# Kernel tuning notes

Hardware: AMD Instinct MI355X
Metric: run time of the kernel (lower is better)

## Reference

```python
import jax, jax.numpy as jnp
import numpy as np

GCN_DIM, GEO_DIM, HIDDEN_DIM, TOWER_DIM, RECENT_K = 128, 32, 256, 128, 50
NUM_ITEMS, NUM_USERS = 100000, 16384


def _normalize(x, eps=1e-12):
    # torch F.normalize(dim=1): x / max(||x||, eps)
    n = jnp.linalg.norm(x, axis=1, keepdims=True)
    return x / jnp.maximum(n, eps)


def setup_inputs() -> dict:
    key = jax.random.key(0)
    ks = jax.random.split(key, 16)
    s = 0.05  # weight init scale
    return {
        "item_feat": jax.random.normal(ks[0], (NUM_ITEMS, 2), jnp.float32),
        "gcn_item_emb": jax.random.normal(ks[1], (NUM_ITEMS, GCN_DIM), jnp.float32),
        "gcn_user_emb": jax.random.normal(ks[2], (NUM_USERS, GCN_DIM), jnp.float32),
        "user_items": jax.random.randint(ks[3], (NUM_USERS, RECENT_K), 0, NUM_ITEMS, jnp.int32),
        "Wg": s * jax.random.normal(ks[4], (2, GEO_DIM), jnp.float32),
        "bg": jnp.zeros((GEO_DIM,), jnp.float32),
        "Wi1": s * jax.random.normal(ks[5], (GCN_DIM + GEO_DIM, HIDDEN_DIM), jnp.float32),
        "bi1": jnp.zeros((HIDDEN_DIM,), jnp.float32),
        "Wi2": s * jax.random.normal(ks[6], (HIDDEN_DIM, TOWER_DIM), jnp.float32),
        "bi2": jnp.zeros((TOWER_DIM,), jnp.float32),
        "Wq": s * jax.random.normal(ks[7], (GCN_DIM, TOWER_DIM), jnp.float32),
        "bq": jnp.zeros((TOWER_DIM,), jnp.float32),
        "Wk": s * jax.random.normal(ks[8], (TOWER_DIM, TOWER_DIM), jnp.float32),
        "bk": jnp.zeros((TOWER_DIM,), jnp.float32),
        "Wu1": s * jax.random.normal(ks[9], (GCN_DIM + TOWER_DIM, HIDDEN_DIM), jnp.float32),
        "bu1": jnp.zeros((HIDDEN_DIM,), jnp.float32),
        "Wu2": s * jax.random.normal(ks[10], (HIDDEN_DIM, TOWER_DIM), jnp.float32),
        "bu2": jnp.zeros((TOWER_DIM,), jnp.float32),
    }


def reference(item_feat, gcn_item_emb, gcn_user_emb, user_items,
              Wg, bg, Wi1, bi1, Wi2, bi2, Wq, bq, Wk, bk, Wu1, bu1, Wu2, bu2):
    # ---- encode_items ----
    geo = jax.nn.relu(item_feat @ Wg + bg)                       # [I, GEO]
    xi = jnp.concatenate([geo, gcn_item_emb], axis=1)            # [I, GEO+GCN]
    item_emb = _normalize(jax.nn.relu(xi @ Wi1 + bi1) @ Wi2 + bi2)  # [I, T]

    # ---- encode_users (batched ragged attention pooling) ----
    h = item_emb[user_items]                                     # [U, K, T] gather
    q = gcn_user_emb @ Wq + bq                                   # [U, T]
    k = h @ Wk + bk                                              # [U, K, T]
    scores = jnp.einsum('ut,ukt->uk', q, k)                      # [U, K]
    alpha = jax.nn.softmax(scores, axis=1)                       # softmax over history
    rep = jnp.einsum('uk,ukt->ut', alpha, h)                     # [U, T]
    fused = jnp.concatenate([gcn_user_emb, rep], axis=1)         # [U, GCN+T]
    user_emb = _normalize(jax.nn.relu(fused @ Wu1 + bu1) @ Wu2 + bu2)  # [U, T]

    return jnp.concatenate([item_emb, user_emb], axis=0)         # [I+U, T]
```

## Files before the change

kernel.cpp:

```cpp
#include <hip/hip_runtime.h>
#include <hip/hip_bf16.h>
#include <math.h>

#define NITEMS 100000
#define NUSERS 16384
#define GCN 128
#define GEO 32
#define HIDD 256
#define TD 128
#define RK 50

typedef unsigned int uint;
typedef unsigned short ushort;
typedef __bf16 bf16x8 __attribute__((ext_vector_type(8)));
typedef float f32x4 __attribute__((ext_vector_type(4)));

__device__ __forceinline__ ushort bfb(float x) {
  union { __hip_bfloat16 b; ushort u; } t; t.b = __float2bfloat16(x); return t.u;
}
__device__ __forceinline__ uint packbf2(float a, float b) {
  return (uint)bfb(a) | ((uint)bfb(b) << 16);
}
__device__ __forceinline__ float bflo(uint d) { return __uint_as_float(d << 16); }
__device__ __forceinline__ float bfhi(uint d) { return __uint_as_float(d & 0xffff0000u); }

union U4B { uint4 u; bf16x8 b; };
__device__ __forceinline__ bf16x8 ldfrag(const ushort* p) { U4B t; t.u = *(const uint4*)p; return t.b; }
__device__ __forceinline__ bf16x8 pack8c(float4 a0, float4 a1) {
  bf16x8 r;
  r[0] = (__bf16)a0.x; r[1] = (__bf16)a0.y; r[2] = (__bf16)a0.z; r[3] = (__bf16)a0.w;
  r[4] = (__bf16)a1.x; r[5] = (__bf16)a1.y; r[6] = (__bf16)a1.z; r[7] = (__bf16)a1.w;
  return r;
}

__global__ __launch_bounds__(256) void prep_all(
    const float* __restrict__ Wi1, const float* __restrict__ Wi2,
    const float* __restrict__ Wu1, const float* __restrict__ Wu2,
    const float* __restrict__ Wq, const float* __restrict__ Wk,
    const float* __restrict__ bq, const float* __restrict__ gcn_item,
    ushort* __restrict__ Wi1P, ushort* __restrict__ Wi2P,
    ushort* __restrict__ Wu1P, ushort* __restrict__ Wu2P,
    float* __restrict__ WqkS, float* __restrict__ bqk,
    ushort* __restrict__ gitemT)
{
  int id = blockIdx.x * 256 + threadIdx.x;
  if (id < 40960) {
    int k = id >> 8, c = id & 255;
    Wi1P[(k >> 5) * 8192 + c * 32 + (k & 31)] = bfb(Wi1[id]);
  } else if (id < 73728) {
    int i = id - 40960; int k = i >> 7, c = i & 127;
    Wi2P[(k >> 5) * 4096 + c * 32 + (k & 31)] = bfb(Wi2[i]);
  } else if (id < 139264) {
    int i = id - 73728; int k = i >> 8, c = i & 255;
    Wu1P[(k >> 5) * 8192 + c * 32 + (k & 31)] = bfb(Wu1[i]);
  } else if (id < 172032) {
    int i = id - 139264; int k = i >> 7, c = i & 127;
    Wu2P[(k >> 5) * 4096 + c * 32 + (k & 31)] = bfb(Wu2[i]);
  } else if (id < 188416) {
    int i = id - 172032; int g = i >> 7, s = i & 127;
    float acc = 0.f;
    for (int t = 0; t < 128; t += 4) {
      float4 a = *(const float4*)(Wq + g * 128 + t);
      float4 b = *(const float4*)(Wk + s * 128 + t);
      acc += a.x * b.x + a.y * b.y + a.z * b.z + a.w * b.w;
    }
    WqkS[g * 128 + s] = acc;
  } else if (id < 188544) {
    int s = id - 188416;
    float acc = 0.f;
    for (int t = 0; t < 128; t += 4) {
      float4 a = *(const float4*)(bq + t);
      float4 b = *(const float4*)(Wk + s * 128 + t);
      acc += a.x * b.x + a.y * b.y + a.z * b.z + a.w * b.w;
    }
    bqk[s] = acc;
  } else if (id < 1788544) {
    int u = id - 188544;
    int r = u >> 4, cu = u & 15;
    size_t base = (size_t)r * GCN + cu * 8;
    float4 v0 = *(const float4*)(gcn_item + base);
    float4 v1 = *(const float4*)(gcn_item + base + 4);
    uint4 o;
    o.x = packbf2(v0.x, v0.y); o.y = packbf2(v0.z, v0.w);
    o.z = packbf2(v1.x, v1.y); o.w = packbf2(v1.z, v1.w);
    int kb = cu >> 2, g = cu & 3;
    size_t ou = (((size_t)(r >> 4) * 4 + kb) * 16 + (r & 15)) * 4 + g;
    *(uint4*)(gitemT + ou * 8) = o;
  } else if (id < 1789056) {
    int t = id - 1788544;
    int r = 100000 + (t >> 4), cu = t & 15;
    int kb = cu >> 2, g = cu & 3;
    size_t ou = (((size_t)(r >> 4) * 4 + kb) * 16 + (r & 15)) * 4 + g;
    uint4 z; z.x = 0; z.y = 0; z.z = 0; z.w = 0;
    *(uint4*)(gitemT + ou * 8) = z;
  }
}

__global__ __launch_bounds__(256, 2) void item_mlp(
    const ushort* __restrict__ gitemT, const float* __restrict__ feat,
    const float* __restrict__ Wg, const float* __restrict__ bg,
    const ushort* __restrict__ W1P, const float* __restrict__ b1,
    const ushort* __restrict__ W2P, const float* __restrict__ b2,
    float* __restrict__ outp, ushort* __restrict__ outb)
{
  __shared__ __align__(16) ushort s_h[64 * 264];
  __shared__ float s_red[64 * 4];

  const int tid = threadIdx.x;
  const int wid = tid >> 6, lane = tid & 63, g = lane >> 4, q = lane & 15;
  const int i0 = blockIdx.x * 64;

  bf16x8 afr[4][4];
  #pragma unroll
  for (int kb = 0; kb < 4; ++kb)
    #pragma unroll
    for (int rf = 0; rf < 4; ++rf)
      afr[kb][rf] = ldfrag(gitemT + ((((size_t)(blockIdx.x * 4 + rf) * 4 + kb) * 16 + q) * 4 + g) * 8);

  const ushort* bb1 = W1P + (wid * 64 + q) * 32 + g * 8;
  bf16x8 bfr[5][4];
  #pragma unroll
  for (int kb = 0; kb < 5; ++kb)
    #pragma unroll
    for (int cf = 0; cf < 4; ++cf)
      bfr[kb][cf] = ldfrag(bb1 + kb * 8192 + cf * 512);

  bf16x8 ageo[4];
  {
    const float4 w0a = *(const float4*)(Wg + g * 8),      w0b = *(const float4*)(Wg + g * 8 + 4);
    const float4 w1a = *(const float4*)(Wg + 32 + g * 8), w1b = *(const float4*)(Wg + 32 + g * 8 + 4);
    const float4 ba  = *(const float4*)(bg + g * 8),      bb = *(const float4*)(bg + g * 8 + 4);
    #pragma unroll
    for (int rf = 0; rf < 4; ++rf) {
      int row = i0 + q + 16 * rf;
      if (row > NITEMS - 1) row = NITEMS - 1;
      float2 f = *(const float2*)(feat + 2 * (size_t)row);
      float4 lo, hi;
      lo.x = fmaxf(fmaf(f.x, w0a.x, fmaf(f.y, w1a.x, ba.x)), 0.f);
      lo.y = fmaxf(fmaf(f.x, w0a.y, fmaf(f.y, w1a.y, ba.y)), 0.f);
      lo.z = fmaxf(fmaf(f.x, w0a.z, fmaf(f.y, w1a.z, ba.z)), 0.f);
      lo.w = fmaxf(fmaf(f.x, w0a.w, fmaf(f.y, w1a.w, ba.w)), 0.f);
      hi.x = fmaxf(fmaf(f.x, w0b.x, fmaf(f.y, w1b.x, bb.x)), 0.f);
      hi.y = fmaxf(fmaf(f.x, w0b.y, fmaf(f.y, w1b.y, bb.y)), 0.f);
      hi.z = fmaxf(fmaf(f.x, w0b.z, fmaf(f.y, w1b.z, bb.z)), 0.f);
      hi.w = fmaxf(fmaf(f.x, w0b.w, fmaf(f.y, w1b.w, bb.w)), 0.f);
      ageo[rf] = pack8c(lo, hi);
    }
  }

  f32x4 acc[4][4];
  #pragma unroll
  for (int cf = 0; cf < 4; ++cf) {
    float bv = b1[wid * 64 + cf * 16 + q];
    f32x4 t = {bv, bv, bv, bv};
    #pragma unroll
    for (int rf = 0; rf < 4; ++rf) acc[rf][cf] = t;
  }
  #pragma unroll
  for (int rf = 0; rf < 4; ++rf)
    #pragma unroll
    for (int cf = 0; cf < 4; ++cf)
      acc[rf][cf] = __builtin_amdgcn_mfma_f32_16x16x32_bf16(ageo[rf], bfr[0][cf], acc[rf][cf], 0, 0, 0);
  #pragma unroll
  for (int kb = 0; kb < 4; ++kb)
    #pragma unroll
    for (int rf = 0; rf < 4; ++rf)
      #pragma unroll
      for (int cf = 0; cf < 4; ++cf)
        acc[rf][cf] = __builtin_amdgcn_mfma_f32_16x16x32_bf16(afr[kb][rf], bfr[kb + 1][cf], acc[rf][cf], 0, 0, 0);

  const ushort* bb2 = W2P + (wid * 32 + q) * 32 + g * 8;
  bf16x8 b2f[8][2];
  #pragma unroll
  for (int kb = 0; kb < 8; ++kb)
    #pragma unroll
    for (int cf = 0; cf < 2; ++cf)
      b2f[kb][cf] = ldfrag(bb2 + kb * 4096 + cf * 512);

  #pragma unroll
  for (int rf = 0; rf < 4; ++rf)
    #pragma unroll
    for (int cf = 0; cf < 4; ++cf)
      #pragma unroll
      for (int e = 0; e < 4; ++e)
        s_h[(16 * rf + 4 * g + e) * 264 + wid * 64 + cf * 16 + q] = bfb(fmaxf(acc[rf][cf][e], 0.f));
  __syncthreads();

  f32x4 acc2[4][2];
  #pragma unroll
  for (int cf = 0; cf < 2; ++cf) {
    float bv = b2[wid * 32 + cf * 16 + q];
    f32x4 t = {bv, bv, bv, bv};
    #pragma unroll
    for (int rf = 0; rf < 4; ++rf) acc2[rf][cf] = t;
  }
  #pragma unroll
  for (int kb = 0; kb < 8; ++kb) {
    bf16x8 af[4];
    #pragma unroll
    for (int rf = 0; rf < 4; ++rf) af[rf] = ldfrag(&s_h[(16 * rf + q) * 264 + kb * 32 + g * 8]);
    #pragma unroll
    for (int rf = 0; rf < 4; ++rf)
      #pragma unroll
      for (int cf = 0; cf < 2; ++cf)
        acc2[rf][cf] = __builtin_amdgcn_mfma_f32_16x16x32_bf16(af[rf], b2f[kb][cf], acc2[rf][cf], 0, 0, 0);
  }

  #pragma unroll
  for (int rf = 0; rf < 4; ++rf) {
    #pragma unroll
    for (int e = 0; e < 4; ++e) {
      float p = acc2[rf][0][e] * acc2[rf][0][e] + acc2[rf][1][e] * acc2[rf][1][e];
      p += __shfl_xor(p, 1, 16); p += __shfl_xor(p, 2, 16);
      p += __shfl_xor(p, 4, 16); p += __shfl_xor(p, 8, 16);
      if (q == 0) s_red[(16 * rf + 4 * g + e) * 4 + wid] = p;
    }
  }
  __syncthreads();
  #pragma unroll
  for (int rf = 0; rf < 4; ++rf) {
    #pragma unroll
    for (int e = 0; e < 4; ++e) {
      int row = 16 * rf + 4 * g + e;
      int grow = i0 + row;
      if (grow < NITEMS) {
        float s = s_red[row * 4] + s_red[row * 4 + 1] + s_red[row * 4 + 2] + s_red[row * 4 + 3];
        float sc = 1.f / fmaxf(sqrtf(s), 1e-12f);
        #pragma unroll
        for (int cf = 0; cf < 2; ++cf) {
          float v = acc2[rf][cf][e] * sc;
          outp[(size_t)grow * TD + wid * 32 + cf * 16 + q] = v;
          outb[(size_t)grow * TD + wid * 32 + cf * 16 + q] = bfb(v);
        }
      }
    }
  }
}

__global__ __launch_bounds__(256, 3) void user_mlp(
    const float* __restrict__ gcn_user, const ushort* __restrict__ repB,
    const ushort* __restrict__ W1P, const float* __restrict__ b1,
    const ushort* __restrict__ W2P, const float* __restrict__ b2,
    float* __restrict__ outp)
{
  __shared__ __align__(16) ushort s_h[32 * 264];
  __shared__ float s_red[32 * 4];

  const int tid = threadIdx.x;
  const int wid = tid >> 6, lane = tid & 63, g = lane >> 4, q = lane & 15;
  const int i0 = blockIdx.x * 32;

  bf16x8 auf[8][2];
  #pragma unroll
  for (int kb = 0; kb < 4; ++kb)
    #pragma unroll
    for (int rf = 0; rf < 2; ++rf) {
      const float* rp = gcn_user + (size_t)(i0 + q + 16 * rf) * GCN + kb * 32 + g * 8;
      auf[kb][rf] = pack8c(*(const float4*)rp, *(const float4*)(rp + 4));
    }
  #pragma unroll
  for (int kb = 4; kb < 8; ++kb)
    #pragma unroll
    for (int rf = 0; rf < 2; ++rf)
      auf[kb][rf] = ldfrag(repB + (size_t)(i0 + q + 16 * rf) * TD + (kb - 4) * 32 + g * 8);

  const ushort* bb1 = W1P + (wid * 64 + q) * 32 + g * 8;
  bf16x8 bcur[4];
  #pragma unroll
  for (int cf = 0; cf < 4; ++cf) bcur[cf] = ldfrag(bb1 + cf * 512);

  f32x4 acc[2][4];
  #pragma unroll
  for (int cf = 0; cf < 4; ++cf) {
    float bv = b1[wid * 64 + cf * 16 + q];
    f32x4 t = {bv, bv, bv, bv};
    acc[0][cf] = t; acc[1][cf] = t;
  }
  #pragma unroll
  for (int kb = 0; kb < 8; ++kb) {
    bf16x8 bnxt[4];
    if (kb < 7) {
      #pragma unroll
      for (int cf = 0; cf < 4; ++cf) bnxt[cf] = ldfrag(bb1 + (kb + 1) * 8192 + cf * 512);
    }
    #pragma unroll
    for (int rf = 0; rf < 2; ++rf)
      #pragma unroll
      for (int cf = 0; cf < 4; ++cf)
        acc[rf][cf] = __builtin_amdgcn_mfma_f32_16x16x32_bf16(auf[kb][rf], bcur[cf], acc[rf][cf], 0, 0, 0);
    if (kb < 7) {
      #pragma unroll
      for (int cf = 0; cf < 4; ++cf) bcur[cf] = bnxt[cf];
    }
  }

  const ushort* bb2 = W2P + (wid * 32 + q) * 32 + g * 8;
  bf16x8 b2f[8][2];
  #pragma unroll
  for (int kb = 0; kb < 8; ++kb)
    #pragma unroll
    for (int cf = 0; cf < 2; ++cf)
      b2f[kb][cf] = ldfrag(bb2 + kb * 4096 + cf * 512);

  #pragma unroll
  for (int rf = 0; rf < 2; ++rf)
    #pragma unroll
    for (int cf = 0; cf < 4; ++cf)
      #pragma unroll
      for (int e = 0; e < 4; ++e)
        s_h[(16 * rf + 4 * g + e) * 264 + wid * 64 + cf * 16 + q] = bfb(fmaxf(acc[rf][cf][e], 0.f));
  __syncthreads();

  f32x4 acc2[2][2];
  #pragma unroll
  for (int cf = 0; cf < 2; ++cf) {
    float bv = b2[wid * 32 + cf * 16 + q];
    f32x4 t = {bv, bv, bv, bv};
    acc2[0][cf] = t; acc2[1][cf] = t;
  }
  #pragma unroll
  for (int kb = 0; kb < 8; ++kb) {
    bf16x8 af[2];
    #pragma unroll
    for (int rf = 0; rf < 2; ++rf) af[rf] = ldfrag(&s_h[(16 * rf + q) * 264 + kb * 32 + g * 8]);
    #pragma unroll
    for (int rf = 0; rf < 2; ++rf)
      #pragma unroll
      for (int cf = 0; cf < 2; ++cf)
        acc2[rf][cf] = __builtin_amdgcn_mfma_f32_16x16x32_bf16(af[rf], b2f[kb][cf], acc2[rf][cf], 0, 0, 0);
  }

  #pragma unroll
  for (int rf = 0; rf < 2; ++rf) {
    #pragma unroll
    for (int e = 0; e < 4; ++e) {
      float p = acc2[rf][0][e] * acc2[rf][0][e] + acc2[rf][1][e] * acc2[rf][1][e];
      p += __shfl_xor(p, 1, 16); p += __shfl_xor(p, 2, 16);
      p += __shfl_xor(p, 4, 16); p += __shfl_xor(p, 8, 16);
      if (q == 0) s_red[(16 * rf + 4 * g + e) * 4 + wid] = p;
    }
  }
  __syncthreads();
  #pragma unroll
  for (int rf = 0; rf < 2; ++rf) {
    #pragma unroll
    for (int e = 0; e < 4; ++e) {
      int row = 16 * rf + 4 * g + e;
      float s = s_red[row * 4] + s_red[row * 4 + 1] + s_red[row * 4 + 2] + s_red[row * 4 + 3];
      float sc = 1.f / fmaxf(sqrtf(s), 1e-12f);
      #pragma unroll
      for (int cf = 0; cf < 2; ++cf)
        outp[(size_t)(i0 + row) * TD + wid * 32 + cf * 16 + q] = acc2[rf][cf][e] * sc;
    }
  }
}

__global__ __launch_bounds__(256) void qt_kernel(
    const float* __restrict__ gcn_user, const float* __restrict__ WqkS,
    const float* __restrict__ bqk, float* __restrict__ qt)
{
  __shared__ float s_gue[16 * 132];
  const int tid = threadIdx.x;
  const int u0 = blockIdx.x * 16;
  #pragma unroll
  for (int r = 0; r < 8; ++r) {
    int lin = r * 256 + tid;
    int u = lin >> 7, c = lin & 127;
    s_gue[u * 132 + c] = gcn_user[(size_t)(u0 + u) * GCN + c];
  }
  __syncthreads();
  const int ul = tid >> 4, tx = tid & 15, c0 = tx * 8;
  float a[8];
  { float4 b4 = *(const float4*)(bqk + c0); float4 b5 = *(const float4*)(bqk + c0 + 4);
    a[0]=b4.x; a[1]=b4.y; a[2]=b4.z; a[3]=b4.w; a[4]=b5.x; a[5]=b5.y; a[6]=b5.z; a[7]=b5.w; }
  for (int g = 0; g < 128; ++g) {
    float x = s_gue[ul * 132 + g];
    float4 w4 = *(const float4*)(WqkS + g * 128 + c0);
    float4 w5 = *(const float4*)(WqkS + g * 128 + c0 + 4);
    a[0] = fmaf(x, w4.x, a[0]); a[1] = fmaf(x, w4.y, a[1]);
    a[2] = fmaf(x, w4.z, a[2]); a[3] = fmaf(x, w4.w, a[3]);
    a[4] = fmaf(x, w5.x, a[4]); a[5] = fmaf(x, w5.y, a[5]);
    a[6] = fmaf(x, w5.z, a[6]); a[7] = fmaf(x, w5.w, a[7]);
  }
  float* op = qt + (size_t)(u0 + ul) * TD + c0;
  *(float4*)op = make_float4(a[0], a[1], a[2], a[3]);
  *(float4*)(op + 4) = make_float4(a[4], a[5], a[6], a[7]);
}

__global__ __launch_bounds__(256) void attn_kernel(
    const int* __restrict__ user_items, const float* __restrict__ qt,
    const ushort* __restrict__ itemB, ushort* __restrict__ repB)
{
  __shared__ int s_idx[4][52];
  const int tid = threadIdx.x;
  const int wid = tid >> 6, lane = tid & 63, g = lane >> 4, q = lane & 15;
  const int u = blockIdx.x * 4 + wid;
  const int c0 = q * 8;

  if (lane < 52) s_idx[wid][lane] = (lane < 50) ? user_items[(size_t)u * RK + lane] : 0;
  float qv[8];
  { float4 a = *(const float4*)(qt + (size_t)u * TD + c0);
    float4 b = *(const float4*)(qt + (size_t)u * TD + c0 + 4);
    qv[0]=a.x; qv[1]=a.y; qv[2]=a.z; qv[3]=a.w; qv[4]=b.x; qv[5]=b.y; qv[6]=b.z; qv[7]=b.w; }

  uint4 h[13]; float sc[13];
  #pragma unroll
  for (int i = 0; i < 13; ++i) {
    int j = 4 * i + g;
    int idx = s_idx[wid][j];
    h[i] = *(const uint4*)(itemB + (size_t)idx * TD + c0);
    float p = bflo(h[i].x) * qv[0] + bfhi(h[i].x) * qv[1]
            + bflo(h[i].y) * qv[2] + bfhi(h[i].y) * qv[3]
            + bflo(h[i].z) * qv[4] + bfhi(h[i].z) * qv[5]
            + bflo(h[i].w) * qv[6] + bfhi(h[i].w) * qv[7];
    p += __shfl_xor(p, 1, 16); p += __shfl_xor(p, 2, 16);
    p += __shfl_xor(p, 4, 16); p += __shfl_xor(p, 8, 16);
    sc[i] = (j < RK) ? p : -3.0e38f;
  }
  float m = sc[0];
  #pragma unroll
  for (int i = 1; i < 13; ++i) m = fmaxf(m, sc[i]);
  m = fmaxf(m, __shfl_xor(m, 16, 64));
  m = fmaxf(m, __shfl_xor(m, 32, 64));
  float ssum = 0.f;
  #pragma unroll
  for (int i = 0; i < 13; ++i) { sc[i] = __expf(sc[i] - m); ssum += sc[i]; }
  ssum += __shfl_xor(ssum, 16, 64);
  ssum += __shfl_xor(ssum, 32, 64);
  const float inv = 1.f / ssum;
  float rep[8] = {0, 0, 0, 0, 0, 0, 0, 0};
  #pragma unroll
  for (int i = 0; i < 13; ++i) {
    float a = sc[i] * inv;
    rep[0] = fmaf(a, bflo(h[i].x), rep[0]); rep[1] = fmaf(a, bfhi(h[i].x), rep[1]);
    rep[2] = fmaf(a, bflo(h[i].y), rep[2]); rep[3] = fmaf(a, bfhi(h[i].y), rep[3]);
    rep[4] = fmaf(a, bflo(h[i].z), rep[4]); rep[5] = fmaf(a, bfhi(h[i].z), rep[5]);
    rep[6] = fmaf(a, bflo(h[i].w), rep[6]); rep[7] = fmaf(a, bfhi(h[i].w), rep[7]);
  }
  #pragma unroll
  for (int c = 0; c < 8; ++c) {
    rep[c] += __shfl_xor(rep[c], 16, 64);
    rep[c] += __shfl_xor(rep[c], 32, 64);
  }
  if (g == 0) {
    uint4 o;
    o.x = packbf2(rep[0], rep[1]); o.y = packbf2(rep[2], rep[3]);
    o.z = packbf2(rep[4], rep[5]); o.w = packbf2(rep[6], rep[7]);
    *(uint4*)(repB + (size_t)u * TD + c0) = o;
  }
}

extern "C" void kernel_launch(void* const* d_in, const int* in_sizes, int n_in,
                              void* d_out, int out_size, void* d_ws, size_t ws_size,
                              hipStream_t stream) {
  const float* item_feat  = (const float*)d_in[0];
  const float* gcn_item   = (const float*)d_in[1];
  const float* gcn_user   = (const float*)d_in[2];
  const int*   user_items = (const int*)  d_in[3];
  const float* Wg  = (const float*)d_in[4];
  const float* bg  = (const float*)d_in[5];
  const float* Wi1 = (const float*)d_in[6];
  const float* bi1 = (const float*)d_in[7];
  const float* Wi2 = (const float*)d_in[8];
  const float* bi2 = (const float*)d_in[9];
  const float* Wq  = (const float*)d_in[10];
  const float* bq  = (const float*)d_in[11];
  const float* Wk  = (const float*)d_in[12];
  const float* Wu1 = (const float*)d_in[14];
  const float* bu1 = (const float*)d_in[15];
  const float* Wu2 = (const float*)d_in[16];
  const float* bu2 = (const float*)d_in[17];
  float* out = (float*)d_out;

  char* ws = (char*)d_ws;
  ushort* Wi1P   = (ushort*)(ws + 0);
  ushort* Wi2P   = (ushort*)(ws + 81920);
  ushort* Wu1P   = (ushort*)(ws + 147456);
  ushort* Wu2P   = (ushort*)(ws + 278528);
  float*  WqkS   = (float*) (ws + 344064);
  float*  bqk    = (float*) (ws + 409600);
  float*  qtb    = (float*) (ws + 410112);
  ushort* gitemT = (ushort*)(ws + 8798720);
  ushort* itemB  = (ushort*)(ws + 34406912);
  ushort* repB   = (ushort*)(ws + 60006912);

  prep_all<<<6989, 256, 0, stream>>>(Wi1, Wi2, Wu1, Wu2, Wq, Wk, bq, gcn_item,
                                     Wi1P, Wi2P, Wu1P, Wu2P, WqkS, bqk, gitemT);
  item_mlp<<<(NITEMS + 63) / 64, 256, 0, stream>>>(
      gitemT, item_feat, Wg, bg, Wi1P, bi1, Wi2P, bi2, out, itemB);
  qt_kernel<<<NUSERS / 16, 256, 0, stream>>>(gcn_user, WqkS, bqk, qtb);
  attn_kernel<<<NUSERS / 4, 256, 0, stream>>>(user_items, qtb, itemB, repB);
  user_mlp<<<NUSERS / 32, 256, 0, stream>>>(
      gcn_user, repB, Wu1P, bu1, Wu2P, bu2, out + (size_t)NITEMS * TD);
}
```

Before: 140.7 us.

## Fuse attention pooling into user MLP and precompute geo features in prep

```diff
diff --git a/kernel.cpp b/kernel.cpp
--- a/kernel.cpp
+++ b/kernel.cpp
@@ -9,6 +9,7 @@
 #define HIDD 256
 #define TD 128
 #define RK 50
+#define NRB 6252
 
 typedef unsigned int uint;
 typedef unsigned short ushort;
@@ -38,6 +39,8 @@
     const float* __restrict__ Wu1, const float* __restrict__ Wu2,
     const float* __restrict__ Wq, const float* __restrict__ Wk,
     const float* __restrict__ bq, const float* __restrict__ gcn_item,
+    const float* __restrict__ feat, const float* __restrict__ Wg,
+    const float* __restrict__ bg,
     ushort* __restrict__ Wi1P, ushort* __restrict__ Wi2P,
     ushort* __restrict__ Wu1P, ushort* __restrict__ Wu2P,
     float* __restrict__ WqkS, float* __restrict__ bqk,
@@ -83,22 +86,43 @@
     uint4 o;
     o.x = packbf2(v0.x, v0.y); o.y = packbf2(v0.z, v0.w);
     o.z = packbf2(v1.x, v1.y); o.w = packbf2(v1.z, v1.w);
-    int kb = cu >> 2, g = cu & 3;
-    size_t ou = (((size_t)(r >> 4) * 4 + kb) * 16 + (r & 15)) * 4 + g;
-    *(uint4*)(gitemT + ou * 8) = o;
-  } else if (id < 1789056) {
+    int kb = 1 + (cu >> 2), g = cu & 3;
+    size_t ou = ((size_t)(r >> 4) * 5 + kb) * 512 + (r & 15) * 32 + g * 8;
+    *(uint4*)(gitemT + ou) = o;
+  } else if (id < 2188672) {
     int t = id - 1788544;
+    int r = t >> 2, gg = t & 3;
+    int fr = (r < NITEMS) ? r : (NITEMS - 1);
+    float2 f = *(const float2*)(feat + 2 * (size_t)fr);
+    const float4 w0a = *(const float4*)(Wg + gg * 8),      w0b = *(const float4*)(Wg + gg * 8 + 4);
+    const float4 w1a = *(const float4*)(Wg + 32 + gg * 8), w1b = *(const float4*)(Wg + 32 + gg * 8 + 4);
+    const float4 ba  = *(const float4*)(bg + gg * 8),      bb = *(const float4*)(bg + gg * 8 + 4);
+    float4 lo, hi;
+    lo.x = fmaxf(fmaf(f.x, w0a.x, fmaf(f.y, w1a.x, ba.x)), 0.f);
+    lo.y = fmaxf(fmaf(f.x, w0a.y, fmaf(f.y, w1a.y, ba.y)), 0.f);
+    lo.z = fmaxf(fmaf(f.x, w0a.z, fmaf(f.y, w1a.z, ba.z)), 0.f);
+    lo.w = fmaxf(fmaf(f.x, w0a.w, fmaf(f.y, w1a.w, ba.w)), 0.f);
+    hi.x = fmaxf(fmaf(f.x, w0b.x, fmaf(f.y, w1b.x, bb.x)), 0.f);
+    hi.y = fmaxf(fmaf(f.x, w0b.y, fmaf(f.y, w1b.y, bb.y)), 0.f);
+    hi.z = fmaxf(fmaf(f.x, w0b.z, fmaf(f.y, w1b.z, bb.z)), 0.f);
+    hi.w = fmaxf(fmaf(f.x, w0b.w, fmaf(f.y, w1b.w, bb.w)), 0.f);
+    uint4 o;
+    o.x = packbf2(lo.x, lo.y); o.y = packbf2(lo.z, lo.w);
+    o.z = packbf2(hi.x, hi.y); o.w = packbf2(hi.z, hi.w);
+    size_t ou = ((size_t)(r >> 4) * 5) * 512 + (r & 15) * 32 + gg * 8;
+    *(uint4*)(gitemT + ou) = o;
+  } else if (id < 2189184) {
+    int t = id - 2188672;
     int r = 100000 + (t >> 4), cu = t & 15;
-    int kb = cu >> 2, g = cu & 3;
-    size_t ou = (((size_t)(r >> 4) * 4 + kb) * 16 + (r & 15)) * 4 + g;
+    int kb = 1 + (cu >> 2), g = cu & 3;
+    size_t ou = ((size_t)(r >> 4) * 5 + kb) * 512 + (r & 15) * 32 + g * 8;
     uint4 z; z.x = 0; z.y = 0; z.z = 0; z.w = 0;
-    *(uint4*)(gitemT + ou * 8) = z;
+    *(uint4*)(gitemT + ou) = z;
   }
 }
 
 __global__ __launch_bounds__(256, 2) void item_mlp(
-    const ushort* __restrict__ gitemT, const float* __restrict__ feat,
-    const float* __restrict__ Wg, const float* __restrict__ bg,
+    const ushort* __restrict__ gitemT,
     const ushort* __restrict__ W1P, const float* __restrict__ b1,
     const ushort* __restrict__ W2P, const float* __restrict__ b2,
     float* __restrict__ outp, ushort* __restrict__ outb)
@@ -110,12 +134,12 @@
   const int wid = tid >> 6, lane = tid & 63, g = lane >> 4, q = lane & 15;
   const int i0 = blockIdx.x * 64;
 
-  bf16x8 afr[4][4];
-  #pragma unroll
-  for (int kb = 0; kb < 4; ++kb)
+  bf16x8 afr[5][4];
+  #pragma unroll
+  for (int kb = 0; kb < 5; ++kb)
     #pragma unroll
     for (int rf = 0; rf < 4; ++rf)
-      afr[kb][rf] = ldfrag(gitemT + ((((size_t)(blockIdx.x * 4 + rf) * 4 + kb) * 16 + q) * 4 + g) * 8);
+      afr[kb][rf] = ldfrag(gitemT + ((size_t)(blockIdx.x * 4 + rf) * 5 + kb) * 512 + q * 32 + g * 8);
 
   const ushort* bb1 = W1P + (wid * 64 + q) * 32 + g * 8;
   bf16x8 bfr[5][4];
@@ -124,29 +148,6 @@
     #pragma unroll
     for (int cf = 0; cf < 4; ++cf)
       bfr[kb][cf] = ldfrag(bb1 + kb * 8192 + cf * 512);
-
-  bf16x8 ageo[4];
-  {
-    const float4 w0a = *(const float4*)(Wg + g * 8),      w0b = *(const float4*)(Wg + g * 8 + 4);
-    const float4 w1a = *(const float4*)(Wg + 32 + g * 8), w1b = *(const float4*)(Wg + 32 + g * 8 + 4);
-    const float4 ba  = *(const float4*)(bg + g * 8),      bb = *(const float4*)(bg + g * 8 + 4);
-    #pragma unroll
-    for (int rf = 0; rf < 4; ++rf) {
-      int row = i0 + q + 16 * rf;
-      if (row > NITEMS - 1) row = NITEMS - 1;
-      float2 f = *(const float2*)(feat + 2 * (size_t)row);
-      float4 lo, hi;
-      lo.x = fmaxf(fmaf(f.x, w0a.x, fmaf(f.y, w1a.x, ba.x)), 0.f);
-      lo.y = fmaxf(fmaf(f.x, w0a.y, fmaf(f.y, w1a.y, ba.y)), 0.f);
-      lo.z = fmaxf(fmaf(f.x, w0a.z, fmaf(f.y, w1a.z, ba.z)), 0.f);
-      lo.w = fmaxf(fmaf(f.x, w0a.w, fmaf(f.y, w1a.w, ba.w)), 0.f);
-      hi.x = fmaxf(fmaf(f.x, w0b.x, fmaf(f.y, w1b.x, bb.x)), 0.f);
-      hi.y = fmaxf(fmaf(f.x, w0b.y, fmaf(f.y, w1b.y, bb.y)), 0.f);
-      hi.z = fmaxf(fmaf(f.x, w0b.z, fmaf(f.y, w1b.z, bb.z)), 0.f);
-      hi.w = fmaxf(fmaf(f.x, w0b.w, fmaf(f.y, w1b.w, bb.w)), 0.f);
-      ageo[rf] = pack8c(lo, hi);
-    }
-  }
 
   f32x4 acc[4][4];
   #pragma unroll
@@ -157,17 +158,12 @@
     for (int rf = 0; rf < 4; ++rf) acc[rf][cf] = t;
   }
   #pragma unroll
-  for (int rf = 0; rf < 4; ++rf)
-    #pragma unroll
-    for (int cf = 0; cf < 4; ++cf)
-      acc[rf][cf] = __builtin_amdgcn_mfma_f32_16x16x32_bf16(ageo[rf], bfr[0][cf], acc[rf][cf], 0, 0, 0);
-  #pragma unroll
-  for (int kb = 0; kb < 4; ++kb)
+  for (int kb = 0; kb < 5; ++kb)
     #pragma unroll
     for (int rf = 0; rf < 4; ++rf)
       #pragma unroll
       for (int cf = 0; cf < 4; ++cf)
-        acc[rf][cf] = __builtin_amdgcn_mfma_f32_16x16x32_bf16(afr[kb][rf], bfr[kb + 1][cf], acc[rf][cf], 0, 0, 0);
+        acc[rf][cf] = __builtin_amdgcn_mfma_f32_16x16x32_bf16(afr[kb][rf], bfr[kb][cf], acc[rf][cf], 0, 0, 0);
 
   const ushort* bb2 = W2P + (wid * 32 + q) * 32 + g * 8;
   bf16x8 b2f[8][2];
@@ -237,127 +233,9 @@
   }
 }
 
-__global__ __launch_bounds__(256, 3) void user_mlp(
-    const float* __restrict__ gcn_user, const ushort* __restrict__ repB,
-    const ushort* __restrict__ W1P, const float* __restrict__ b1,
-    const ushort* __restrict__ W2P, const float* __restrict__ b2,
-    float* __restrict__ outp)
-{
-  __shared__ __align__(16) ushort s_h[32 * 264];
-  __shared__ float s_red[32 * 4];
-
-  const int tid = threadIdx.x;
-  const int wid = tid >> 6, lane = tid & 63, g = lane >> 4, q = lane & 15;
-  const int i0 = blockIdx.x * 32;
-
-  bf16x8 auf[8][2];
-  #pragma unroll
-  for (int kb = 0; kb < 4; ++kb)
-    #pragma unroll
-    for (int rf = 0; rf < 2; ++rf) {
-      const float* rp = gcn_user + (size_t)(i0 + q + 16 * rf) * GCN + kb * 32 + g * 8;
-      auf[kb][rf] = pack8c(*(const float4*)rp, *(const float4*)(rp + 4));
-    }
-  #pragma unroll
-  for (int kb = 4; kb < 8; ++kb)
-    #pragma unroll
-    for (int rf = 0; rf < 2; ++rf)
-      auf[kb][rf] = ldfrag(repB + (size_t)(i0 + q + 16 * rf) * TD + (kb - 4) * 32 + g * 8);
-
-  const ushort* bb1 = W1P + (wid * 64 + q) * 32 + g * 8;
-  bf16x8 bcur[4];
-  #pragma unroll
-  for (int cf = 0; cf < 4; ++cf) bcur[cf] = ldfrag(bb1 + cf * 512);
-
-  f32x4 acc[2][4];
-  #pragma unroll
-  for (int cf = 0; cf < 4; ++cf) {
-    float bv = b1[wid * 64 + cf * 16 + q];
-    f32x4 t = {bv, bv, bv, bv};
-    acc[0][cf] = t; acc[1][cf] = t;
-  }
-  #pragma unroll
-  for (int kb = 0; kb < 8; ++kb) {
-    bf16x8 bnxt[4];
-    if (kb < 7) {
-      #pragma unroll
-      for (int cf = 0; cf < 4; ++cf) bnxt[cf] = ldfrag(bb1 + (kb + 1) * 8192 + cf * 512);
-    }
-    #pragma unroll
-    for (int rf = 0; rf < 2; ++rf)
-      #pragma unroll
-      for (int cf = 0; cf < 4; ++cf)
-        acc[rf][cf] = __builtin_amdgcn_mfma_f32_16x16x32_bf16(auf[kb][rf], bcur[cf], acc[rf][cf], 0, 0, 0);
-    if (kb < 7) {
-      #pragma unroll
-      for (int cf = 0; cf < 4; ++cf) bcur[cf] = bnxt[cf];
-    }
-  }
-
-  const ushort* bb2 = W2P + (wid * 32 + q) * 32 + g * 8;
-  bf16x8 b2f[8][2];
-  #pragma unroll
-  for (int kb = 0; kb < 8; ++kb)
-    #pragma unroll
-    for (int cf = 0; cf < 2; ++cf)
-      b2f[kb][cf] = ldfrag(bb2 + kb * 4096 + cf * 512);
-
-  #pragma unroll
-  for (int rf = 0; rf < 2; ++rf)
-    #pragma unroll
-    for (int cf = 0; cf < 4; ++cf)
-      #pragma unroll
-      for (int e = 0; e < 4; ++e)
-        s_h[(16 * rf + 4 * g + e) * 264 + wid * 64 + cf * 16 + q] = bfb(fmaxf(acc[rf][cf][e], 0.f));
-  __syncthreads();
-
-  f32x4 acc2[2][2];
-  #pragma unroll
-  for (int cf = 0; cf < 2; ++cf) {
-    float bv = b2[wid * 32 + cf * 16 + q];
-    f32x4 t = {bv, bv, bv, bv};
-    acc2[0][cf] = t; acc2[1][cf] = t;
-  }
-  #pragma unroll
-  for (int kb = 0; kb < 8; ++kb) {
-    bf16x8 af[2];
-    #pragma unroll
-    for (int rf = 0; rf < 2; ++rf) af[rf] = ldfrag(&s_h[(16 * rf + q) * 264 + kb * 32 + g * 8]);
-    #pragma unroll
-    for (int rf = 0; rf < 2; ++rf)
-      #pragma unroll
-      for (int cf = 0; cf < 2; ++cf)
-        acc2[rf][cf] = __builtin_amdgcn_mfma_f32_16x16x32_bf16(af[rf], b2f[kb][cf], acc2[rf][cf], 0, 0, 0);
-  }
-
-  #pragma unroll
-  for (int rf = 0; rf < 2; ++rf) {
-    #pragma unroll
-    for (int e = 0; e < 4; ++e) {
-      float p = acc2[rf][0][e] * acc2[rf][0][e] + acc2[rf][1][e] * acc2[rf][1][e];
-      p += __shfl_xor(p, 1, 16); p += __shfl_xor(p, 2, 16);
-      p += __shfl_xor(p, 4, 16); p += __shfl_xor(p, 8, 16);
-      if (q == 0) s_red[(16 * rf + 4 * g + e) * 4 + wid] = p;
-    }
-  }
-  __syncthreads();
-  #pragma unroll
-  for (int rf = 0; rf < 2; ++rf) {
-    #pragma unroll
-    for (int e = 0; e < 4; ++e) {
-      int row = 16 * rf + 4 * g + e;
-      float s = s_red[row * 4] + s_red[row * 4 + 1] + s_red[row * 4 + 2] + s_red[row * 4 + 3];
-      float sc = 1.f / fmaxf(sqrtf(s), 1e-12f);
-      #pragma unroll
-      for (int cf = 0; cf < 2; ++cf)
-        outp[(size_t)(i0 + row) * TD + wid * 32 + cf * 16 + q] = acc2[rf][cf][e] * sc;
-    }
-  }
-}
-
 __global__ __launch_bounds__(256) void qt_kernel(
     const float* __restrict__ gcn_user, const float* __restrict__ WqkS,
-    const float* __restrict__ bqk, float* __restrict__ qt)
+    const float* __restrict__ bqk, ushort* __restrict__ qtb)
 {
   __shared__ float s_gue[16 * 132];
   const int tid = threadIdx.x;
@@ -382,71 +260,179 @@
     a[4] = fmaf(x, w5.x, a[4]); a[5] = fmaf(x, w5.y, a[5]);
     a[6] = fmaf(x, w5.z, a[6]); a[7] = fmaf(x, w5.w, a[7]);
   }
-  float* op = qt + (size_t)(u0 + ul) * TD + c0;
-  *(float4*)op = make_float4(a[0], a[1], a[2], a[3]);
-  *(float4*)(op + 4) = make_float4(a[4], a[5], a[6], a[7]);
-}
-
-__global__ __launch_bounds__(256) void attn_kernel(
-    const int* __restrict__ user_items, const float* __restrict__ qt,
-    const ushort* __restrict__ itemB, ushort* __restrict__ repB)
+  uint4 o;
+  o.x = packbf2(a[0], a[1]); o.y = packbf2(a[2], a[3]);
+  o.z = packbf2(a[4], a[5]); o.w = packbf2(a[6], a[7]);
+  *(uint4*)(qtb + (size_t)(u0 + ul) * TD + c0) = o;
+}
+
+__global__ __launch_bounds__(512, 4) void users_fused(
+    const int* __restrict__ user_items, const ushort* __restrict__ qtb,
+    const ushort* __restrict__ itemB, const float* __restrict__ gcn_user,
+    const ushort* __restrict__ W1P, const float* __restrict__ b1,
+    const ushort* __restrict__ W2P, const float* __restrict__ b2,
+    float* __restrict__ outp)
 {
-  __shared__ int s_idx[4][52];
+  __shared__ int s_idx[8][52];
+  __shared__ __align__(16) ushort s_rep[32][136];
+  __shared__ __align__(16) ushort s_h[32 * 264];
+  __shared__ float s_red[32 * 4];
+
   const int tid = threadIdx.x;
   const int wid = tid >> 6, lane = tid & 63, g = lane >> 4, q = lane & 15;
-  const int u = blockIdx.x * 4 + wid;
+  const int u0 = blockIdx.x * 32;
   const int c0 = q * 8;
 
-  if (lane < 52) s_idx[wid][lane] = (lane < 50) ? user_items[(size_t)u * RK + lane] : 0;
-  float qv[8];
-  { float4 a = *(const float4*)(qt + (size_t)u * TD + c0);
-    float4 b = *(const float4*)(qt + (size_t)u * TD + c0 + 4);
-    qv[0]=a.x; qv[1]=a.y; qv[2]=a.z; qv[3]=a.w; qv[4]=b.x; qv[5]=b.y; qv[6]=b.z; qv[7]=b.w; }
-
-  uint4 h[13]; float sc[13];
-  #pragma unroll
-  for (int i = 0; i < 13; ++i) {
-    int j = 4 * i + g;
-    int idx = s_idx[wid][j];
-    h[i] = *(const uint4*)(itemB + (size_t)idx * TD + c0);
-    float p = bflo(h[i].x) * qv[0] + bfhi(h[i].x) * qv[1]
-            + bflo(h[i].y) * qv[2] + bfhi(h[i].y) * qv[3]
-            + bflo(h[i].z) * qv[4] + bfhi(h[i].z) * qv[5]
-            + bflo(h[i].w) * qv[6] + bfhi(h[i].w) * qv[7];
+  for (int w = 0; w < 4; ++w) {
+    const int lu = w * 8 + wid;
+    const int u = u0 + lu;
+    if (lane < 52) s_idx[wid][lane] = (lane < 50) ? user_items[(size_t)u * RK + lane] : 0;
+    float qv[8];
+    { uint4 a = *(const uint4*)(qtb + (size_t)u * TD + c0);
+      qv[0]=bflo(a.x); qv[1]=bfhi(a.x); qv[2]=bflo(a.y); qv[3]=bfhi(a.y);
+      qv[4]=bflo(a.z); qv[5]=bfhi(a.z); qv[6]=bflo(a.w); qv[7]=bfhi(a.w); }
+
+    uint4 h[13]; float sc[13];
+    #pragma unroll
+    for (int i = 0; i < 13; ++i) {
+      int j = 4 * i + g;
+      int idx = s_idx[wid][j];
+      h[i] = *(const uint4*)(itemB + (size_t)idx * TD + c0);
+      float p = bflo(h[i].x) * qv[0] + bfhi(h[i].x) * qv[1]
+              + bflo(h[i].y) * qv[2] + bfhi(h[i].y) * qv[3]
+              + bflo(h[i].z) * qv[4] + bfhi(h[i].z) * qv[5]
+              + bflo(h[i].w) * qv[6] + bfhi(h[i].w) * qv[7];
+      p += __shfl_xor(p, 1, 16); p += __shfl_xor(p, 2, 16);
+      p += __shfl_xor(p, 4, 16); p += __shfl_xor(p, 8, 16);
+      sc[i] = (j < RK) ? p : -3.0e38f;
+    }
+    float m = sc[0];
+    #pragma unroll
+    for (int i = 1; i < 13; ++i) m = fmaxf(m, sc[i]);
+    m = fmaxf(m, __shfl_xor(m, 16, 64));
+    m = fmaxf(m, __shfl_xor(m, 32, 64));
+    float ssum = 0.f;
+    #pragma unroll
+    for (int i = 0; i < 13; ++i) { sc[i] = __expf(sc[i] - m); ssum += sc[i]; }
+    ssum += __shfl_xor(ssum, 16, 64);
+    ssum += __shfl_xor(ssum, 32, 64);
+    const float inv = 1.f / ssum;
+    float rep[8] = {0, 0, 0, 0, 0, 0, 0, 0};
+    #pragma unroll
+    for (int i = 0; i < 13; ++i) {
+      float a = sc[i] * inv;
+      rep[0] = fmaf(a, bflo(h[i].x), rep[0]); rep[1] = fmaf(a, bfhi(h[i].x), rep[1]);
+      rep[2] = fmaf(a, bflo(h[i].y), rep[2]); rep[3] = fmaf(a, bfhi(h[i].y), rep[3]);
+      rep[4] = fmaf(a, bflo(h[i].z), rep[4]); rep[5] = fmaf(a, bfhi(h[i].z), rep[5]);
+      rep[6] = fmaf(a, bflo(h[i].w), rep[6]); rep[7] = fmaf(a, bfhi(h[i].w), rep[7]);
+    }
+    #pragma unroll
+    for (int c = 0; c < 8; ++c) {
+      rep[c] += __shfl_xor(rep[c], 16, 64);
+      rep[c] += __shfl_xor(rep[c], 32, 64);
+    }
+    if (g == 0) {
+      uint4 o;
+      o.x = packbf2(rep[0], rep[1]); o.y = packbf2(rep[2], rep[3]);
+      o.z = packbf2(rep[4], rep[5]); o.w = packbf2(rep[6], rep[7]);
+      *(uint4*)(&s_rep[lu][c0]) = o;
+    }
+  }
+  __syncthreads();
+
+  const int rg = wid >> 2, cg = wid & 3;
+  const int r0 = rg * 16;
+
+  bf16x8 a1[8];
+  #pragma unroll
+  for (int kb = 0; kb < 4; ++kb) {
+    const float* rp = gcn_user + (size_t)(u0 + r0 + q) * GCN + kb * 32 + g * 8;
+    a1[kb] = pack8c(*(const float4*)rp, *(const float4*)(rp + 4));
+  }
+  #pragma unroll
+  for (int kb = 4; kb < 8; ++kb)
+    a1[kb] = ldfrag(&s_rep[r0 + q][(kb - 4) * 32 + g * 8]);
+
+  const ushort* bb1 = W1P + (cg * 64 + q) * 32 + g * 8;
+  bf16x8 bcur[4];
+  #pragma unroll
+  for (int cf = 0; cf < 4; ++cf) bcur[cf] = ldfrag(bb1 + cf * 512);
+
+  f32x4 acc[4];
+  #pragma unroll
+  for (int cf = 0; cf < 4; ++cf) {
+    float bv = b1[cg * 64 + cf * 16 + q];
+    f32x4 t = {bv, bv, bv, bv};
+    acc[cf] = t;
+  }
+  #pragma unroll
+  for (int kb = 0; kb < 8; ++kb) {
+    bf16x8 bnxt[4];
+    if (kb < 7) {
+      #pragma unroll
+      for (int cf = 0; cf < 4; ++cf) bnxt[cf] = ldfrag(bb1 + (kb + 1) * 8192 + cf * 512);
+    }
+    #pragma unroll
+    for (int cf = 0; cf < 4; ++cf)
+      acc[cf] = __builtin_amdgcn_mfma_f32_16x16x32_bf16(a1[kb], bcur[cf], acc[cf], 0, 0, 0);
+    if (kb < 7) {
+      #pragma unroll
+      for (int cf = 0; cf < 4; ++cf) bcur[cf] = bnxt[cf];
+    }
+  }
+
+  #pragma unroll
+  for (int cf = 0; cf < 4; ++cf)
+    #pragma unroll
+    for (int e = 0; e < 4; ++e)
+      s_h[(r0 + 4 * g + e) * 264 + cg * 64 + cf * 16 + q] = bfb(fmaxf(acc[cf][e], 0.f));
+  __syncthreads();
+
+  const ushort* bb2 = W2P + (cg * 32 + q) * 32 + g * 8;
+  bf16x8 b2cur[2];
+  #pragma unroll
+  for (int cf = 0; cf < 2; ++cf) b2cur[cf] = ldfrag(bb2 + cf * 512);
+
+  f32x4 acc2[2];
+  #pragma unroll
+  for (int cf = 0; cf < 2; ++cf) {
+    float bv = b2[cg * 32 + cf * 16 + q];
+    f32x4 t = {bv, bv, bv, bv};
+    acc2[cf] = t;
+  }
+  #pragma unroll
+  for (int kb = 0; kb < 8; ++kb) {
+    bf16x8 bnxt[2];
+    if (kb < 7) {
+      #pragma unroll
+      for (int cf = 0; cf < 2; ++cf) bnxt[cf] = ldfrag(bb2 + (kb + 1) * 4096 + cf * 512);
+    }
+    bf16x8 af = ldfrag(&s_h[(r0 + q) * 264 + kb * 32 + g * 8]);
+    #pragma unroll
+    for (int cf = 0; cf < 2; ++cf)
+      acc2[cf] = __builtin_amdgcn_mfma_f32_16x16x32_bf16(af, b2cur[cf], acc2[cf], 0, 0, 0);
+    if (kb < 7) {
+      #pragma unroll
+      for (int cf = 0; cf < 2; ++cf) b2cur[cf] = bnxt[cf];
+    }
+  }
+
+  #pragma unroll
+  for (int e = 0; e < 4; ++e) {
+    float p = acc2[0][e] * acc2[0][e] + acc2[1][e] * acc2[1][e];
     p += __shfl_xor(p, 1, 16); p += __shfl_xor(p, 2, 16);
     p += __shfl_xor(p, 4, 16); p += __shfl_xor(p, 8, 16);
-    sc[i] = (j < RK) ? p : -3.0e38f;
-  }
-  float m = sc[0];
-  #pragma unroll
-  for (int i = 1; i < 13; ++i) m = fmaxf(m, sc[i]);
-  m = fmaxf(m, __shfl_xor(m, 16, 64));
-  m = fmaxf(m, __shfl_xor(m, 32, 64));
-  float ssum = 0.f;
-  #pragma unroll
-  for (int i = 0; i < 13; ++i) { sc[i] = __expf(sc[i] - m); ssum += sc[i]; }
-  ssum += __shfl_xor(ssum, 16, 64);
-  ssum += __shfl_xor(ssum, 32, 64);
-  const float inv = 1.f / ssum;
-  float rep[8] = {0, 0, 0, 0, 0, 0, 0, 0};
-  #pragma unroll
-  for (int i = 0; i < 13; ++i) {
-    float a = sc[i] * inv;
-    rep[0] = fmaf(a, bflo(h[i].x), rep[0]); rep[1] = fmaf(a, bfhi(h[i].x), rep[1]);
-    rep[2] = fmaf(a, bflo(h[i].y), rep[2]); rep[3] = fmaf(a, bfhi(h[i].y), rep[3]);
-    rep[4] = fmaf(a, bflo(h[i].z), rep[4]); rep[5] = fmaf(a, bfhi(h[i].z), rep[5]);
-    rep[6] = fmaf(a, bflo(h[i].w), rep[6]); rep[7] = fmaf(a, bfhi(h[i].w), rep[7]);
-  }
-  #pragma unroll
-  for (int c = 0; c < 8; ++c) {
-    rep[c] += __shfl_xor(rep[c], 16, 64);
-    rep[c] += __shfl_xor(rep[c], 32, 64);
-  }
-  if (g == 0) {
-    uint4 o;
-    o.x = packbf2(rep[0], rep[1]); o.y = packbf2(rep[2], rep[3]);
-    o.z = packbf2(rep[4], rep[5]); o.w = packbf2(rep[6], rep[7]);
-    *(uint4*)(repB + (size_t)u * TD + c0) = o;
+    if (q == 0) s_red[(r0 + 4 * g + e) * 4 + cg] = p;
+  }
+  __syncthreads();
+  #pragma unroll
+  for (int e = 0; e < 4; ++e) {
+    int row = r0 + 4 * g + e;
+    float s = s_red[row * 4] + s_red[row * 4 + 1] + s_red[row * 4 + 2] + s_red[row * 4 + 3];
+    float sc = 1.f / fmaxf(sqrtf(s), 1e-12f);
+    #pragma unroll
+    for (int cf = 0; cf < 2; ++cf)
+      outp[(size_t)(u0 + row) * TD + cg * 32 + cf * 16 + q] = acc2[cf][e] * sc;
   }
 }
 
@@ -479,17 +465,17 @@
   ushort* Wu2P   = (ushort*)(ws + 278528);
   float*  WqkS   = (float*) (ws + 344064);
   float*  bqk    = (float*) (ws + 409600);
-  float*  qtb    = (float*) (ws + 410112);
-  ushort* gitemT = (ushort*)(ws + 8798720);
-  ushort* itemB  = (ushort*)(ws + 34406912);
-  ushort* repB   = (ushort*)(ws + 60006912);
-
-  prep_all<<<6989, 256, 0, stream>>>(Wi1, Wi2, Wu1, Wu2, Wq, Wk, bq, gcn_item,
+  ushort* qtb    = (ushort*)(ws + 410112);
+  ushort* gitemT = (ushort*)(ws + 4604416);
+  ushort* itemB  = (ushort*)(ws + 36614656);
+
+  prep_all<<<8552, 256, 0, stream>>>(Wi1, Wi2, Wu1, Wu2, Wq, Wk, bq, gcn_item,
+                                     item_feat, Wg, bg,
                                      Wi1P, Wi2P, Wu1P, Wu2P, WqkS, bqk, gitemT);
   item_mlp<<<(NITEMS + 63) / 64, 256, 0, stream>>>(
-      gitemT, item_feat, Wg, bg, Wi1P, bi1, Wi2P, bi2, out, itemB);
+      gitemT, Wi1P, bi1, Wi2P, bi2, out, itemB);
   qt_kernel<<<NUSERS / 16, 256, 0, stream>>>(gcn_user, WqkS, bqk, qtb);
-  attn_kernel<<<NUSERS / 4, 256, 0, stream>>>(user_items, qtb, itemB, repB);
-  user_mlp<<<NUSERS / 32, 256, 0, stream>>>(
-      gcn_user, repB, Wu1P, bu1, Wu2P, bu2, out + (size_t)NITEMS * TD);
-}
+  users_fused<<<NUSERS / 32, 512, 0, stream>>>(
+      user_items, qtb, itemB, gcn_user, Wu1P, bu1, Wu2P, bu2,
+      out + (size_t)NITEMS * TD);
+}
```

After: 180.7 us. 1.28x slower.
